# Performance work log

Measured on AMD Instinct MI355X. Metric: run time of the kernel, lower is better.

Reference implementation:

```python
import jax, jax.numpy as jnp
import numpy as np

B, SZ_C, S, D_KV, H_DIM = 2048, 8, 32, 32, 512
NEG = B // 4  # batchsize > 64 branch
TEMP = 0.5
EPS = 1e-8
BN_EPS = 1e-5


def setup_inputs() -> dict:
    key = jax.random.key(0)
    ks = jax.random.split(key, 8)
    x = jax.random.normal(ks[0], (B, SZ_C, S, D_KV), dtype=jnp.float32)
    W1 = jax.random.normal(ks[1], (H_DIM, D_KV), dtype=jnp.float32) * 0.05
    b1 = jnp.zeros((H_DIM,), jnp.float32)
    gamma = jnp.ones((H_DIM,), jnp.float32)
    beta = jnp.zeros((H_DIM,), jnp.float32)
    W2 = jax.random.normal(ks[2], (D_KV, H_DIM), dtype=jnp.float32) * 0.05
    b2 = jnp.zeros((D_KV,), jnp.float32)
    fcW = jax.random.normal(ks[3], (32, S * D_KV), dtype=jnp.float32) * 0.03
    fcb = jnp.zeros((32,), jnp.float32)
    # negatives: raw draws in [0, B-1); shifted past the self index inside reference
    neg_idx = jax.random.randint(ks[4], (B, NEG), 0, B - 1, dtype=jnp.int32)
    return {"x": x, "W1": W1, "b1": b1, "gamma": gamma, "beta": beta,
            "W2": W2, "b2": b2, "fcW": fcW, "fcb": fcb, "neg_idx": neg_idx}


def reference(x, W1, b1, gamma, beta, W2, b2, fcW, fcb, neg_idx):
    # per-channel MLP with training-mode BatchNorm (stats over the B*S rows of each channel)
    xc = jnp.transpose(x, (1, 0, 2, 3)).reshape(SZ_C, B * S, D_KV)   # [C, N, d_kv]
    h = jnp.einsum('cnd,hd->cnh', xc, W1) + b1                        # [C, N, h]
    mu = jnp.mean(h, axis=1, keepdims=True)
    var = jnp.mean((h - mu) ** 2, axis=1, keepdims=True)              # biased, as BN
    h = jax.nn.relu((h - mu) * jax.lax.rsqrt(var + BN_EPS) * gamma + beta)
    y = jnp.einsum('cnh,dh->cnd', h, W2) + b2                         # [C, N, d_kv]
    y = y.reshape(SZ_C, B, S * D_KV)                                  # raw flatten == torch views
    Zc = jnp.einsum('cbf,of->cbo', y, fcW) + fcb                      # [C, B, 32]
    Z = jnp.transpose(Zc, (1, 0, 2))                                  # [B, C, 32]

    Zn = Z / jnp.clip(jnp.linalg.norm(Z, axis=-1, keepdims=True), EPS, None)

    # shift raw draws in [0, B-1) past i -> uniform over indices != i
    idx = neg_idx + (neg_idx >= jnp.arange(B, dtype=neg_idx.dtype)[:, None]).astype(neg_idx.dtype)
    neg = Zn[idx]                                                     # [B, NEG, C, 32]
    neg_sim = jnp.einsum('bcd,bncd->bn', Zn, neg) / SZ_C              # mean over channels

    # mean pairwise cosine similarity across channels (j < k)
    G = jnp.einsum('bjd,bkd->bjk', Zn, Zn)                            # [B, C, C]
    mask = jnp.triu(jnp.ones((SZ_C, SZ_C), bool), 1)
    num_comb = SZ_C * (SZ_C - 1) // 2
    pos_sim = jnp.where(mask, G, 0.0).sum(axis=(1, 2)) / num_comb     # [B]

    l = jnp.exp(pos_sim / TEMP) / jnp.sum(jnp.exp(neg_sim / TEMP), axis=1)  # [B]
    Z_out = jnp.mean(Z, axis=1)                                       # [B, 32]
    return Z_out, l
```

## Files before the change

kernel.cpp:

```cpp
#include <hip/hip_runtime.h>
#include <hip/hip_bf16.h>
#include <math.h>

#define NB 2048
#define NC 8
#define NNEG 512

typedef __attribute__((ext_vector_type(8))) short bf16x8;
typedef __attribute__((ext_vector_type(4))) float f32x4;
typedef __attribute__((ext_vector_type(16))) float f32x16;

static __device__ __forceinline__ unsigned short f2b(float f) {
  __hip_bfloat16 h = __float2bfloat16(f);
  return *reinterpret_cast<unsigned short*>(&h);
}
static __device__ __forceinline__ unsigned int pack_rn(float a, float b) {
  unsigned int ua = __float_as_uint(a) + 0x8000u;
  unsigned int ub = __float_as_uint(b) + 0x8000u;
  return __builtin_amdgcn_perm(ub, ua, 0x07060302u);
}
#define MF16(a, b, c) __builtin_amdgcn_mfma_f32_16x16x32_bf16((a), (b), (c), 0, 0, 0)

#define WS_SSUM   0
#define WS_SPROD  256
#define WS_B1EFF  8448
#define WS_Z      12544
#define WS_POS    536832
#define WS_W1B    538880
#define WS_W2B    604416
#define WS_FCWB   612608
#define WS_ZNB    628992
#define WS_SSUMP  891136

__global__ __launch_bounds__(256) void k_stats(const float* __restrict__ x,
                        float* __restrict__ SsumP, float* __restrict__ SprodP) {
  int c = blockIdx.y;
  int t = threadIdx.x;
  int w = t >> 6, l = t & 63;
  int col = l & 31, half = l >> 5;
  f32x16 acc;
  #pragma unroll
  for (int r = 0; r < 16; ++r) acc[r] = 0.f;
  float ssum = 0.f;
  #pragma unroll 2
  for (int i = 0; i < 16; ++i) {
    int chunk = blockIdx.x * 64 + i * 4 + w;
    int b = chunk >> 1;
    int sb = (chunk & 1) * 16 + half * 8;
    const float* base = x + ((size_t)(b * NC + c)) * 1024 + sb * 32 + col;
    float v0 = base[0],   v1 = base[32],  v2 = base[64],  v3 = base[96];
    float v4 = base[128], v5 = base[160], v6 = base[192], v7 = base[224];
    ssum += ((v0 + v1) + (v2 + v3)) + ((v4 + v5) + (v6 + v7));
    uint4 fq;
    fq.x = pack_rn(v0, v1); fq.y = pack_rn(v2, v3);
    fq.z = pack_rn(v4, v5); fq.w = pack_rn(v6, v7);
    bf16x8 f = __builtin_bit_cast(bf16x8, fq);
    acc = __builtin_amdgcn_mfma_f32_32x32x16_bf16(f, f, acc, 0, 0, 0);
  }
  __shared__ float pr[4][1024];
  __shared__ float sred[4][32];
  #pragma unroll
  for (int r = 0; r < 16; ++r) {
    int row = (r & 3) + 8 * (r >> 2) + 4 * half;
    pr[w][row * 32 + col] = acc[r];
  }
  float sv = ssum + __shfl_xor(ssum, 32);
  if (l < 32) sred[w][l] = sv;
  __syncthreads();
  #pragma unroll
  for (int p = 0; p < 4; ++p) {
    int cell = t + p * 256;
    SprodP[((size_t)(c * 64 + blockIdx.x)) * 1024 + cell] =
        (pr[0][cell] + pr[1][cell]) + (pr[2][cell] + pr[3][cell]);
  }
  if (t < 32)
    SsumP[(c * 64 + blockIdx.x) * 32 + t] =
        (sred[0][t] + sred[1][t]) + (sred[2][t] + sred[3][t]);
}

__global__ void k_red(const float* __restrict__ SprodP, const float* __restrict__ SsumP,
                      float* __restrict__ Sprod, float* __restrict__ Ssum) {
  if (blockIdx.x < 32) {
    int g = blockIdx.x * 256 + threadIdx.x;
    int c = g >> 10, cell = g & 1023;
    float s = 0.f;
    #pragma unroll 8
    for (int p = 0; p < 64; ++p)
      s += SprodP[((size_t)(c * 64 + p)) * 1024 + cell];
    Sprod[g] = s;
  } else {
    int t = threadIdx.x;
    int c = t >> 5, d = t & 31;
    float s = 0.f;
    #pragma unroll 8
    for (int p = 0; p < 64; ++p)
      s += SsumP[(c * 64 + p) * 32 + d];
    Ssum[t] = s;
  }
}

__global__ void k_foldcvt(const float* __restrict__ W1, const float* __restrict__ b1,
                       const float* __restrict__ gamma, const float* __restrict__ beta,
                       const float* __restrict__ Ssum, const float* __restrict__ Sprod,
                       const float* __restrict__ W2, const float* __restrict__ fcW,
                       unsigned short* __restrict__ W1B, float* __restrict__ b1eff,
                       unsigned short* __restrict__ W2B, unsigned short* __restrict__ fcWB) {
  if (blockIdx.x >= 16) {
    int j = (blockIdx.x - 16) * 256 + threadIdx.x;
    if (j < 8192)
      ((unsigned int*)W2B)[j] = pack_rn(W2[2 * j], W2[2 * j + 1]);
    ((unsigned int*)fcWB)[j] = pack_rn(fcW[2 * j], fcW[2 * j + 1]);
    return;
  }
  int g = blockIdx.x * 256 + threadIdx.x;
  int c = g >> 9, h = g & 511;
  const float invN = 1.0f / (float)(NB * 32);
  float w[32];
  #pragma unroll
  for (int d = 0; d < 32; ++d) w[d] = W1[h * 32 + d];
  const float* M = Sprod + c * 1024;
  float q = 0.f;
  for (int j = 0; j < 32; ++j) {
    float v = 0.f;
    #pragma unroll
    for (int i2 = 0; i2 < 32; ++i2) v = fmaf(w[i2], M[i2 * 32 + j], v);
    q = fmaf(v, w[j], q);
  }
  float wmu = 0.f;
  #pragma unroll
  for (int d = 0; d < 32; ++d) wmu = fmaf(w[d], Ssum[c * 32 + d] * invN, wmu);
  float bb = b1[h];
  float mean = wmu + bb;
  float e2 = q * invN + 2.f * bb * wmu + bb * bb;
  float var = e2 - mean * mean;
  float alpha = gamma[h] * rsqrtf(var + 1e-5f);
  unsigned int* W1Bu = (unsigned int*)&W1B[((size_t)c * 512 + h) * 32];
  #pragma unroll
  for (int d = 0; d < 16; ++d)
    W1Bu[d] = pack_rn(w[2 * d] * alpha, w[2 * d + 1] * alpha);
  b1eff[c * 512 + h] = (bb - mean) * alpha + beta[h];
}

__global__ __launch_bounds__(256, 2) void k_main(
    const float* __restrict__ x, const unsigned short* __restrict__ W1B,
    const float* __restrict__ b1eff, const unsigned short* __restrict__ W2B,
    const float* __restrict__ b2, const unsigned short* __restrict__ fcWB,
    const float* __restrict__ fcb, float* __restrict__ Z) {
  int c = blockIdx.y;
  int bt0 = blockIdx.x * 4;
  int t = threadIdx.x;
  int w = t >> 6, l = t & 63;
  int lr = l & 15, lg = l >> 4;

  __shared__ unsigned int rbuf[4][64][20];
  __shared__ float zred[2][8][32];

  const unsigned short* W1c = W1B + (size_t)c * 512 * 32;
  const float* b1e = b1eff + c * 512;
  unsigned int* rbw = &rbuf[w][0][0];

  bf16x8 wfR[2];   f32x4 biasR[2];   bf16x8 w2fR[2];   bf16x8 hfreg[4];
  bf16x8 xf[4], xfN[4];

#define LOADX(dst, bti) \
  _Pragma("unroll") for (int sb = 0; sb < 4; ++sb) { \
    int bl = 2 * w + (sb >> 1); \
    int s = (sb & 1) * 16 + lr; \
    const float* src = x + (((size_t)((bti) * 8 + bl) * NC + c) * 32 + s) * 32 + lg * 8; \
    float4 v0 = ((const float4*)src)[0]; \
    float4 v1 = ((const float4*)src)[1]; \
    uint4 fq; \
    fq.x = pack_rn(v0.x, v0.y); fq.y = pack_rn(v0.z, v0.w); \
    fq.z = pack_rn(v1.x, v1.y); fq.w = pack_rn(v1.z, v1.w); \
    dst[sb] = __builtin_bit_cast(bf16x8, fq); \
  }

#define LDWF0() { \
    wfR[0]  = *(const bf16x8*)&W1c[(size_t)lr * 32 + lg * 8]; \
    wfR[1]  = *(const bf16x8*)&W1c[(size_t)(16 + lr) * 32 + lg * 8]; \
    biasR[0] = *(const f32x4*)(b1e + lg * 4); \
    biasR[1] = *(const f32x4*)(b1e + 16 + lg * 4); }

#define GEMM1(dfr) \
  _Pragma("unroll") for (int hb = 0; hb < 2; ++hb) \
  _Pragma("unroll") for (int sb = 0; sb < 4; ++sb) \
    dfr[hb][sb] = MF16(wfR[hb], xf[sb], biasR[hb]);

#define GEMM2() \
  _Pragma("unroll") for (int mb = 0; mb < 4; ++mb) { \
    yacc[mb][0] = MF16(w2fR[0], hfreg[mb], yacc[mb][0]); \
    yacc[mb][1] = MF16(w2fR[1], hfreg[mb], yacc[mb][1]); \
  }

#define PACKWRITE(dfr) \
  _Pragma("unroll") for (int hb = 0; hb < 2; ++hb) \
  _Pragma("unroll") for (int sb = 0; sb < 4; ++sb) { \
    uint2 pk; \
    pk.x = pack_rn(fmaxf(dfr[hb][sb][0], 0.f), fmaxf(dfr[hb][sb][1], 0.f)); \
    pk.y = pack_rn(fmaxf(dfr[hb][sb][2], 0.f), fmaxf(dfr[hb][sb][3], 0.f)); \
    *(uint2*)&rbw[(sb * 16 + lr) * 20 + hb * 8 + lg * 2] = pk; \
  }

#define LOADW(ch) { \
    if ((ch) < 15) { \
      int h1 = ((ch) + 1) * 32; \
      wfR[0]  = *(const bf16x8*)&W1c[(size_t)(h1 + lr) * 32 + lg * 8]; \
      wfR[1]  = *(const bf16x8*)&W1c[(size_t)(h1 + 16 + lr) * 32 + lg * 8]; \
      biasR[0] = *(const f32x4*)(b1e + h1 + lg * 4); \
      biasR[1] = *(const f32x4*)(b1e + h1 + 16 + lg * 4); \
    } \
    w2fR[0] = *(const bf16x8*)&W2B[(size_t)lr * 512 + (ch) * 32 + lg * 8]; \
    w2fR[1] = *(const bf16x8*)&W2B[(size_t)(16 + lr) * 512 + (ch) * 32 + lg * 8]; \
  }

#define READH() \
  _Pragma("unroll") for (int mb = 0; mb < 4; ++mb) \
    hfreg[mb] = *(const bf16x8*)&rbw[(mb * 16 + lr) * 20 + lg * 4];

  LOADX(xf, bt0);
  LDWF0();

  for (int tt = 0; tt < 4; ++tt) {
    int bt = bt0 + tt;

    f32x4 yacc[4][2];
    #pragma unroll
    for (int db = 0; db < 2; ++db) {
      f32x4 bv = *((const f32x4*)(b2 + db * 16 + lg * 4));
      #pragma unroll
      for (int mb = 0; mb < 4; ++mb) yacc[mb][db] = bv;
    }

    {
      f32x4 dfr[2][4];
      GEMM1(dfr);
      PACKWRITE(dfr);
      LOADW(0);
      READH();
    }
    #pragma unroll 3
    for (int ch = 1; ch < 16; ++ch) {
      f32x4 dfr[2][4];
      GEMM1(dfr);
      GEMM2();
      PACKWRITE(dfr);
      LOADW(ch);
      READH();
    }
    GEMM2();

    if (tt < 3) LOADX(xfN, bt + 1);
    LDWF0();

    #pragma unroll
    for (int mb = 0; mb < 4; ++mb) {
      #pragma unroll
      for (int db = 0; db < 2; ++db) {
        uint2 pk;
        pk.x = pack_rn(yacc[mb][db][0], yacc[mb][db][1]);
        pk.y = pack_rn(yacc[mb][db][2], yacc[mb][db][3]);
        *(uint2*)&rbw[(mb * 16 + lr) * 20 + db * 8 + lg * 2] = pk;
      }
    }
    __syncthreads();

    {
      int nt = w & 1, kh = w >> 1;
      int arow = (lr < 8) ? lr : 7;
      const unsigned int* ybase = &rbuf[arow >> 1][(arow & 1) * 32][0];
      f32x4 zacc = {0.f, 0.f, 0.f, 0.f};
      #pragma unroll
      for (int ks = 0; ks < 16; ++ks) {
        int s = kh * 16 + ks;
        uint4 av = *(const uint4*)&ybase[s * 20 + lg * 4];
        bf16x8 afc = __builtin_bit_cast(bf16x8, av);
        bf16x8 bfc = *(const bf16x8*)&fcWB[(size_t)(nt * 16 + lr) * 1024 + s * 32 + lg * 8];
        zacc = MF16(afc, bfc, zacc);
      }
      if (lg < 2) {
        #pragma unroll
        for (int r = 0; r < 4; ++r) zred[kh][lg * 4 + r][nt * 16 + lr] = zacc[r];
      }
    }
    __syncthreads();
    {
      int bloc = t >> 5, o = t & 31;
      Z[((size_t)(bt * 8 + bloc) * NC + c) * 32 + o] =
          zred[0][bloc][o] + zred[1][bloc][o] + fcb[o];
    }
    if (tt < 3) {
      #pragma unroll
      for (int sb = 0; sb < 4; ++sb) xf[sb] = xfN[sb];
    }
  }
#undef LOADX
#undef LDWF0
#undef GEMM1
#undef GEMM2
#undef PACKWRITE
#undef LOADW
#undef READH
}

__global__ void k_znorm(const float* __restrict__ Z, unsigned short* __restrict__ Znb,
                        float* __restrict__ possim, float* __restrict__ out) {
  int b = blockIdx.x;
  int t = threadIdx.x;
  float v = Z[(size_t)b * 256 + t];
  float n2 = v * v;
  #pragma unroll
  for (int m = 16; m >= 1; m >>= 1) n2 += __shfl_xor(n2, m, 64);
  float nrm = fmaxf(sqrtf(n2), 1e-8f);
  float zn = v / nrm;
  Znb[(size_t)b * 256 + t] = f2b(zn);
  __shared__ float sz[256];
  __shared__ float szn[256];
  sz[t] = v; szn[t] = zn;
  __syncthreads();
  if (t < 32) {
    float s = 0.f;
    #pragma unroll
    for (int cc = 0; cc < 8; ++cc) s += sz[cc * 32 + t];
    out[(size_t)b * 32 + t] = s * 0.125f;
    float sd = 0.f, t1 = 0.f;
    #pragma unroll
    for (int cc = 0; cc < 8; ++cc) {
      float z2 = szn[cc * 32 + t];
      sd += z2; t1 = fmaf(z2, z2, t1);
    }
    float t2 = sd * sd;
    #pragma unroll
    for (int m = 16; m >= 1; m >>= 1) {
      t2 += __shfl_xor(t2, m, 64);
      t1 += __shfl_xor(t1, m, 64);
    }
    if (t == 0) possim[b] = (t2 - t1) * 0.5f / 28.0f;
  }
}

__global__ __launch_bounds__(256) void k_negsim(
    const unsigned short* __restrict__ Znb, const int* __restrict__ neg_idx,
    const float* __restrict__ possim, float* __restrict__ lout) {
  int b = blockIdx.x;
  int t = threadIdx.x;
  int w = t >> 6, l = t & 63;
  int lr = l & 15, lg = l >> 4;
  __shared__ uint4 selfv[32];
  __shared__ float rs[4];
  if (t < 32) selfv[t] = ((const uint4*)(Znb + (size_t)b * 256))[t];
  __syncthreads();
  const unsigned short* selfp = (const unsigned short*)selfv;
  const f32x4 fzero = {0.f, 0.f, 0.f, 0.f};
  float esum = 0.f;
  #pragma unroll 2
  for (int mb = 0; mb < 8; ++mb) {
    int m0 = w * 128 + mb * 16;
    int raw = neg_idx[(size_t)b * NNEG + m0 + lr];
    int j = raw + (raw >= b ? 1 : 0);
    const unsigned short* rp = Znb + (size_t)j * 256;
    f32x4 acc = fzero;
    #pragma unroll
    for (int ks = 0; ks < 8; ++ks) {
      bf16x8 af = *(const bf16x8*)(rp + ks * 32 + lg * 8);
      bf16x8 bf = *(const bf16x8*)(selfp + ks * 32 + lg * 8);
      acc = MF16(af, bf, acc);
    }
    if (lr == 0) {
      esum += expf(acc[0] * 0.25f) + expf(acc[1] * 0.25f)
            + expf(acc[2] * 0.25f) + expf(acc[3] * 0.25f);
    }
  }
  #pragma unroll
  for (int m = 32; m >= 1; m >>= 1) esum += __shfl_xor(esum, m, 64);
  if (l == 0) rs[w] = esum;
  __syncthreads();
  if (t == 0) {
    float tot = rs[0] + rs[1] + rs[2] + rs[3];
    lout[b] = expf(possim[b] * 2.0f) / tot;
  }
}

extern "C" void kernel_launch(void* const* d_in, const int* in_sizes, int n_in,
                              void* d_out, int out_size, void* d_ws, size_t ws_size,
                              hipStream_t stream) {
  const float* x     = (const float*)d_in[0];
  const float* W1    = (const float*)d_in[1];
  const float* b1    = (const float*)d_in[2];
  const float* gamma = (const float*)d_in[3];
  const float* beta  = (const float*)d_in[4];
  const float* W2    = (const float*)d_in[5];
  const float* b2    = (const float*)d_in[6];
  const float* fcW   = (const float*)d_in[7];
  const float* fcb   = (const float*)d_in[8];
  const int*   nidx  = (const int*)d_in[9];
  float* ws = (float*)d_ws;
  float* Ssum   = ws + WS_SSUM;
  float* Sprod  = ws + WS_SPROD;
  float* b1eff  = ws + WS_B1EFF;
  float* Z      = ws + WS_Z;
  float* SprodP = ws + WS_Z;
  float* SsumP  = ws + WS_SSUMP;
  float* possim = ws + WS_POS;
  unsigned short* W1Bp  = (unsigned short*)(ws + WS_W1B);
  unsigned short* W2Bp  = (unsigned short*)(ws + WS_W2B);
  unsigned short* fcWBp = (unsigned short*)(ws + WS_FCWB);
  unsigned short* Znbp  = (unsigned short*)(ws + WS_ZNB);
  float* out = (float*)d_out;

  k_stats<<<dim3(64, 8), 256, 0, stream>>>(x, SsumP, SprodP);
  k_red<<<33, 256, 0, stream>>>(SprodP, SsumP, Sprod, Ssum);
  k_foldcvt<<<80, 256, 0, stream>>>(W1, b1, gamma, beta, Ssum, Sprod, W2, fcW,
                                    W1Bp, b1eff, W2Bp, fcWBp);
  k_main<<<dim3(64, 8), 256, 0, stream>>>(x, W1Bp, b1eff, W2Bp, b2, fcWBp, fcb, Z);
  k_znorm<<<NB, 256, 0, stream>>>(Z, Znbp, possim, out);
  k_negsim<<<NB, 256, 0, stream>>>(Znbp, nidx, possim, out + NB * 32);
}
```

Baseline: 170.9 us.

## Merge reduction into fold, fold weight conversion into stats, batch znorm rows

Removes the separate reduction kernel: the fold kernel now sums the per-block partial statistics into shared memory itself, and the W2/fcW bf16 conversion runs on extra blocks of the stats kernel. This cuts one launch and one global round trip. The znorm kernel now handles 8 rows per block with 256 blocks instead of 2048. Negsim prefetches its negative indices and self fragments into registers and splits the MFMA chain into two accumulators for more ILP. The fold step now uses only 16 blocks and each one repeats the 64-way partial reduction, so it has less parallelism than before.

```diff
diff --git a/kernel.cpp b/kernel.cpp
--- a/kernel.cpp
+++ b/kernel.cpp
@@ -21,8 +21,6 @@
 }
 #define MF16(a, b, c) __builtin_amdgcn_mfma_f32_16x16x32_bf16((a), (b), (c), 0, 0, 0)
 
-#define WS_SSUM   0
-#define WS_SPROD  256
 #define WS_B1EFF  8448
 #define WS_Z      12544
 #define WS_POS    536832
@@ -33,7 +31,16 @@
 #define WS_SSUMP  891136
 
 __global__ __launch_bounds__(256) void k_stats(const float* __restrict__ x,
-                        float* __restrict__ SsumP, float* __restrict__ SprodP) {
+                        float* __restrict__ SsumP, float* __restrict__ SprodP,
+                        const float* __restrict__ W2, const float* __restrict__ fcW,
+                        unsigned short* __restrict__ W2B, unsigned short* __restrict__ fcWB) {
+  if (blockIdx.x >= 64) {
+    int g = ((blockIdx.x - 64) * 8 + blockIdx.y) * 256 + threadIdx.x;
+    if (g < 8192)
+      ((unsigned int*)W2B)[g] = pack_rn(W2[2 * g], W2[2 * g + 1]);
+    ((unsigned int*)fcWB)[g] = pack_rn(fcW[2 * g], fcW[2 * g + 1]);
+    return;
+  }
   int c = blockIdx.y;
   int t = threadIdx.x;
   int w = t >> 6, l = t & 63;
@@ -78,57 +85,49 @@
         (sred[0][t] + sred[1][t]) + (sred[2][t] + sred[3][t]);
 }
 
-__global__ void k_red(const float* __restrict__ SprodP, const float* __restrict__ SsumP,
-                      float* __restrict__ Sprod, float* __restrict__ Ssum) {
-  if (blockIdx.x < 32) {
-    int g = blockIdx.x * 256 + threadIdx.x;
-    int c = g >> 10, cell = g & 1023;
+__global__ __launch_bounds__(256) void k_fold(
+    const float* __restrict__ W1, const float* __restrict__ b1,
+    const float* __restrict__ gamma, const float* __restrict__ beta,
+    const float* __restrict__ SsumP, const float* __restrict__ SprodP,
+    unsigned short* __restrict__ W1B, float* __restrict__ b1eff) {
+  int c = blockIdx.x >> 1;
+  int hh = blockIdx.x & 1;
+  int t = threadIdx.x;
+  __shared__ float Ms[1024];
+  __shared__ float Ss[32];
+  #pragma unroll
+  for (int p4 = 0; p4 < 4; ++p4) {
+    int cell = t + p4 * 256;
     float s = 0.f;
     #pragma unroll 8
     for (int p = 0; p < 64; ++p)
       s += SprodP[((size_t)(c * 64 + p)) * 1024 + cell];
-    Sprod[g] = s;
-  } else {
-    int t = threadIdx.x;
-    int c = t >> 5, d = t & 31;
+    Ms[cell] = s;
+  }
+  if (t < 32) {
     float s = 0.f;
     #pragma unroll 8
     for (int p = 0; p < 64; ++p)
-      s += SsumP[(c * 64 + p) * 32 + d];
-    Ssum[t] = s;
-  }
-}
-
-__global__ void k_foldcvt(const float* __restrict__ W1, const float* __restrict__ b1,
-                       const float* __restrict__ gamma, const float* __restrict__ beta,
-                       const float* __restrict__ Ssum, const float* __restrict__ Sprod,
-                       const float* __restrict__ W2, const float* __restrict__ fcW,
-                       unsigned short* __restrict__ W1B, float* __restrict__ b1eff,
-                       unsigned short* __restrict__ W2B, unsigned short* __restrict__ fcWB) {
-  if (blockIdx.x >= 16) {
-    int j = (blockIdx.x - 16) * 256 + threadIdx.x;
-    if (j < 8192)
-      ((unsigned int*)W2B)[j] = pack_rn(W2[2 * j], W2[2 * j + 1]);
-    ((unsigned int*)fcWB)[j] = pack_rn(fcW[2 * j], fcW[2 * j + 1]);
-    return;
-  }
-  int g = blockIdx.x * 256 + threadIdx.x;
-  int c = g >> 9, h = g & 511;
+      s += SsumP[(c * 64 + p) * 32 + t];
+    Ss[t] = s;
+  }
+  __syncthreads();
+
+  int h = hh * 256 + t;
   const float invN = 1.0f / (float)(NB * 32);
   float w[32];
   #pragma unroll
   for (int d = 0; d < 32; ++d) w[d] = W1[h * 32 + d];
-  const float* M = Sprod + c * 1024;
   float q = 0.f;
   for (int j = 0; j < 32; ++j) {
     float v = 0.f;
     #pragma unroll
-    for (int i2 = 0; i2 < 32; ++i2) v = fmaf(w[i2], M[i2 * 32 + j], v);
+    for (int i2 = 0; i2 < 32; ++i2) v = fmaf(w[i2], Ms[i2 * 32 + j], v);
     q = fmaf(v, w[j], q);
   }
   float wmu = 0.f;
   #pragma unroll
-  for (int d = 0; d < 32; ++d) wmu = fmaf(w[d], Ssum[c * 32 + d] * invN, wmu);
+  for (int d = 0; d < 32; ++d) wmu = fmaf(w[d], Ss[d] * invN, wmu);
   float bb = b1[h];
   float mean = wmu + bb;
   float e2 = q * invN + 2.f * bb * wmu + bb * bb;
@@ -302,39 +301,43 @@
 #undef READH
 }
 
-__global__ void k_znorm(const float* __restrict__ Z, unsigned short* __restrict__ Znb,
+__global__ __launch_bounds__(256) void k_znorm(const float* __restrict__ Z,
+                        unsigned short* __restrict__ Znb,
                         float* __restrict__ possim, float* __restrict__ out) {
-  int b = blockIdx.x;
   int t = threadIdx.x;
-  float v = Z[(size_t)b * 256 + t];
-  float n2 = v * v;
-  #pragma unroll
-  for (int m = 16; m >= 1; m >>= 1) n2 += __shfl_xor(n2, m, 64);
-  float nrm = fmaxf(sqrtf(n2), 1e-8f);
-  float zn = v / nrm;
-  Znb[(size_t)b * 256 + t] = f2b(zn);
   __shared__ float sz[256];
   __shared__ float szn[256];
-  sz[t] = v; szn[t] = zn;
-  __syncthreads();
-  if (t < 32) {
-    float s = 0.f;
+  for (int bb = 0; bb < 8; ++bb) {
+    int b = blockIdx.x * 8 + bb;
+    float v = Z[(size_t)b * 256 + t];
+    float n2 = v * v;
     #pragma unroll
-    for (int cc = 0; cc < 8; ++cc) s += sz[cc * 32 + t];
-    out[(size_t)b * 32 + t] = s * 0.125f;
-    float sd = 0.f, t1 = 0.f;
-    #pragma unroll
-    for (int cc = 0; cc < 8; ++cc) {
-      float z2 = szn[cc * 32 + t];
-      sd += z2; t1 = fmaf(z2, z2, t1);
-    }
-    float t2 = sd * sd;
-    #pragma unroll
-    for (int m = 16; m >= 1; m >>= 1) {
-      t2 += __shfl_xor(t2, m, 64);
-      t1 += __shfl_xor(t1, m, 64);
-    }
-    if (t == 0) possim[b] = (t2 - t1) * 0.5f / 28.0f;
+    for (int m = 16; m >= 1; m >>= 1) n2 += __shfl_xor(n2, m, 64);
+    float nrm = fmaxf(sqrtf(n2), 1e-8f);
+    float zn = v / nrm;
+    Znb[(size_t)b * 256 + t] = f2b(zn);
+    sz[t] = v; szn[t] = zn;
+    __syncthreads();
+    if (t < 32) {
+      float s = 0.f;
+      #pragma unroll
+      for (int cc = 0; cc < 8; ++cc) s += sz[cc * 32 + t];
+      out[(size_t)b * 32 + t] = s * 0.125f;
+      float sd = 0.f, t1 = 0.f;
+      #pragma unroll
+      for (int cc = 0; cc < 8; ++cc) {
+        float z2 = szn[cc * 32 + t];
+        sd += z2; t1 = fmaf(z2, z2, t1);
+      }
+      float t2 = sd * sd;
+      #pragma unroll
+      for (int m = 16; m >= 1; m >>= 1) {
+        t2 += __shfl_xor(t2, m, 64);
+        t1 += __shfl_xor(t1, m, 64);
+      }
+      if (t == 0) possim[b] = (t2 - t1) * 0.5f / 28.0f;
+    }
+    __syncthreads();
   }
 }
 
@@ -348,26 +351,31 @@
   __shared__ uint4 selfv[32];
   __shared__ float rs[4];
   if (t < 32) selfv[t] = ((const uint4*)(Znb + (size_t)b * 256))[t];
+  int jA[8];
+  #pragma unroll
+  for (int mb = 0; mb < 8; ++mb) {
+    int raw = neg_idx[(size_t)b * NNEG + w * 128 + mb * 16 + lr];
+    jA[mb] = raw + (raw >= b ? 1 : 0);
+  }
   __syncthreads();
   const unsigned short* selfp = (const unsigned short*)selfv;
+  bf16x8 sf[8];
+  #pragma unroll
+  for (int ks = 0; ks < 8; ++ks) sf[ks] = *(const bf16x8*)(selfp + ks * 32 + lg * 8);
   const f32x4 fzero = {0.f, 0.f, 0.f, 0.f};
   float esum = 0.f;
   #pragma unroll 2
   for (int mb = 0; mb < 8; ++mb) {
-    int m0 = w * 128 + mb * 16;
-    int raw = neg_idx[(size_t)b * NNEG + m0 + lr];
-    int j = raw + (raw >= b ? 1 : 0);
-    const unsigned short* rp = Znb + (size_t)j * 256;
-    f32x4 acc = fzero;
+    const unsigned short* rp = Znb + (size_t)jA[mb] * 256;
+    f32x4 acc0 = fzero, acc1 = fzero;
     #pragma unroll
-    for (int ks = 0; ks < 8; ++ks) {
-      bf16x8 af = *(const bf16x8*)(rp + ks * 32 + lg * 8);
-      bf16x8 bf = *(const bf16x8*)(selfp + ks * 32 + lg * 8);
-      acc = MF16(af, bf, acc);
+    for (int ks = 0; ks < 4; ++ks) {
+      acc0 = MF16(*(const bf16x8*)(rp + ks * 32 + lg * 8), sf[ks], acc0);
+      acc1 = MF16(*(const bf16x8*)(rp + (ks + 4) * 32 + lg * 8), sf[ks + 4], acc1);
     }
     if (lr == 0) {
-      esum += expf(acc[0] * 0.25f) + expf(acc[1] * 0.25f)
-            + expf(acc[2] * 0.25f) + expf(acc[3] * 0.25f);
+      esum += expf((acc0[0] + acc1[0]) * 0.25f) + expf((acc0[1] + acc1[1]) * 0.25f)
+            + expf((acc0[2] + acc1[2]) * 0.25f) + expf((acc0[3] + acc1[3]) * 0.25f);
     }
   }
   #pragma unroll
@@ -394,8 +402,6 @@
   const float* fcb   = (const float*)d_in[8];
   const int*   nidx  = (const int*)d_in[9];
   float* ws = (float*)d_ws;
-  float* Ssum   = ws + WS_SSUM;
-  float* Sprod  = ws + WS_SPROD;
   float* b1eff  = ws + WS_B1EFF;
   float* Z      = ws + WS_Z;
   float* SprodP = ws + WS_Z;
@@ -407,11 +413,9 @@
   unsigned short* Znbp  = (unsigned short*)(ws + WS_ZNB);
   float* out = (float*)d_out;
 
-  k_stats<<<dim3(64, 8), 256, 0, stream>>>(x, SsumP, SprodP);
-  k_red<<<33, 256, 0, stream>>>(SprodP, SsumP, Sprod, Ssum);
-  k_foldcvt<<<80, 256, 0, stream>>>(W1, b1, gamma, beta, Ssum, Sprod, W2, fcW,
-                                    W1Bp, b1eff, W2Bp, fcWBp);
+  k_stats<<<dim3(72, 8), 256, 0, stream>>>(x, SsumP, SprodP, W2, fcW, W2Bp, fcWBp);
+  k_fold<<<16, 256, 0, stream>>>(W1, b1, gamma, beta, SsumP, SprodP, W1Bp, b1eff);
   k_main<<<dim3(64, 8), 256, 0, stream>>>(x, W1Bp, b1eff, W2Bp, b2, fcWBp, fcb, Z);
-  k_znorm<<<NB, 256, 0, stream>>>(Z, Znbp, possim, out);
+  k_znorm<<<256, 256, 0, stream>>>(Z, Znbp, possim, out);
   k_negsim<<<NB, 256, 0, stream>>>(Znbp, nidx, possim, out + NB * 32);
 }
```

Result: slower. 185.1 us (+8.3%).
